# Kernel tuning notes

Measured on AMD Instinct MI355X. Metric: run time of the kernel, lower is better.

Reference implementation:

```python
import jax, jax.numpy as jnp
import numpy as np

TAYLOR_ORDER = 16      # Taylor terms after scaling (||A_s|| <= 0.5 -> machine precision)
MAX_SQUARINGS = 16     # fixed upper bound on squaring steps (jit-friendly)


def batched_expm(A):
    """Vectorized scaling-and-squaring matrix exponential for A of shape [..., n, n].

    Replaces the original per-item torch.linalg.matrix_exp Python loop with one
    fused batched computation (same math: exp(Q*t)).
    """
    n = A.shape[-1]
    I = jnp.eye(n, dtype=A.dtype)
    # per-matrix infinity norm [...,]
    nrm = jnp.max(jnp.sum(jnp.abs(A), axis=-1), axis=-1)
    # number of squarings so that scaled norm <= 0.5
    s = jnp.clip(jnp.ceil(jnp.log2(jnp.maximum(nrm, 1e-30) / 0.5)), 0.0, float(MAX_SQUARINGS))
    As = A * jnp.exp2(-s)[..., None, None]
    # Taylor series: P = I + As + As^2/2! + ...
    P = jnp.broadcast_to(I, A.shape)
    term = P
    for k in range(1, TAYLOR_ORDER + 1):
        term = jnp.matmul(term, As) / k
        P = P + term
    # undo scaling: square s times (data-dependent count via masked squaring)
    s_b = s[..., None, None]
    for i in range(MAX_SQUARINGS):
        P = jnp.where(s_b > i, jnp.matmul(P, P), P)
    return P


def setup_inputs() -> dict:
    key = jax.random.key(0)
    k1, k2 = jax.random.split(key)
    rate_matrix = jax.random.normal(k1, (64, 32768, 4, 4), dtype=jnp.float32)
    time = jax.random.uniform(k2, (64,), dtype=jnp.float32)
    return {"rate_matrix": rate_matrix, "time": time}


def reference(rate_matrix, time):
    # Qt = rate_matrix[i, j] * time[i], batched over (batch, seq_len)
    Qt = rate_matrix * time[:, None, None, None]
    return batched_expm(Qt)  # [B, S, 4, 4] transition probability matrices
```

## Files before the change

### kernel.cpp

```cpp
#include <hip/hip_runtime.h>
#include <math.h>


typedef float f4 __attribute__((ext_vector_type(4)));

constexpr int NMAT = 2;
constexpr int TPB  = 256;
constexpr int MPB  = NMAT * TPB;

__device__ __forceinline__ void mm4(float* __restrict__ D,
                                    const float* __restrict__ X,
                                    const float* __restrict__ Y)
{
    #pragma unroll
    for (int i = 0; i < 4; ++i) {
        const float x0 = X[4*i+0], x1 = X[4*i+1];
        const float x2 = X[4*i+2], x3 = X[4*i+3];
        #pragma unroll
        for (int j = 0; j < 4; ++j) {
            float v = x0 * Y[j];
            v = __builtin_fmaf(x1, Y[4+j],  v);
            v = __builtin_fmaf(x2, Y[8+j],  v);
            v = __builtin_fmaf(x3, Y[12+j], v);
            D[4*i+j] = v;
        }
    }
}

__device__ __forceinline__ void expm4_one(const f4 r[4], float t, f4 o[4])
{
    const float at = fabsf(t);
    float nrm = 0.0f;
    #pragma unroll
    for (int i = 0; i < 4; ++i) {
        float rs = fabsf(r[i].x) + fabsf(r[i].y) + fabsf(r[i].z) + fabsf(r[i].w);
        nrm = fmaxf(nrm, rs);
    }
    nrm *= at;

    float sf = ceilf(log2f(fmaxf(nrm, 1e-30f) * 2.0f));
    sf = fminf(fmaxf(sf, 0.0f), 16.0f);
    const int   si = (int)sf;
    const float c  = t * exp2f(-sf);

    float a[16];
    #pragma unroll
    for (int i = 0; i < 4; ++i) {
        a[4*i+0] = r[i].x * c;
        a[4*i+1] = r[i].y * c;
        a[4*i+2] = r[i].z * c;
        a[4*i+3] = r[i].w * c;
    }

    float A2[16], A3[16];
    mm4(A2, a, a);
    mm4(A3, A2, a);

    constexpr float C2 = 1.0f/2.0f,     C3 = 1.0f/6.0f;
    constexpr float C4 = 1.0f/24.0f,    C5 = 1.0f/120.0f;
    constexpr float C6 = 1.0f/720.0f,   C7 = 1.0f/5040.0f;
    constexpr float C8 = 1.0f/40320.0f, C9 = 1.0f/362880.0f;

    float G[16], HI[16], PI[16];
    #pragma unroll
    for (int i = 0; i < 16; ++i) {
        G[i]  = __builtin_fmaf(C9, A3[i],
                __builtin_fmaf(C8, A2[i], C7 * a[i]));
        HI[i] = __builtin_fmaf(C5, A2[i], C4 * a[i]);
        PI[i] = __builtin_fmaf(C2, A2[i], a[i]);
    }
    G[0]  += C6; G[5]  += C6; G[10] += C6; G[15] += C6;
    HI[0] += C3; HI[5] += C3; HI[10] += C3; HI[15] += C3;
    PI[0] += 1.0f; PI[5] += 1.0f; PI[10] += 1.0f; PI[15] += 1.0f;

    float H[16];
    #pragma unroll
    for (int i = 0; i < 4; ++i) {
        const float g0 = G[4*i+0], g1 = G[4*i+1];
        const float g2 = G[4*i+2], g3 = G[4*i+3];
        #pragma unroll
        for (int j = 0; j < 4; ++j) {
            float v = HI[4*i+j];
            v = __builtin_fmaf(g0, A3[j],    v);
            v = __builtin_fmaf(g1, A3[4+j],  v);
            v = __builtin_fmaf(g2, A3[8+j],  v);
            v = __builtin_fmaf(g3, A3[12+j], v);
            H[4*i+j] = v;
        }
    }

    float P[16];
    #pragma unroll
    for (int i = 0; i < 4; ++i) {
        const float h0 = H[4*i+0], h1 = H[4*i+1];
        const float h2 = H[4*i+2], h3 = H[4*i+3];
        #pragma unroll
        for (int j = 0; j < 4; ++j) {
            float v = PI[4*i+j];
            v = __builtin_fmaf(h0, A3[j],    v);
            v = __builtin_fmaf(h1, A3[4+j],  v);
            v = __builtin_fmaf(h2, A3[8+j],  v);
            v = __builtin_fmaf(h3, A3[12+j], v);
            P[4*i+j] = v;
        }
    }

    int it = si;
    while (it >= 2) {
        float Q[16];
        mm4(Q, P, P);
        mm4(P, Q, Q);
        it -= 2;
    }
    if (it) {
        float Q[16];
        mm4(Q, P, P);
        #pragma unroll
        for (int i = 0; i < 16; ++i) P[i] = Q[i];
    }

    #pragma unroll
    for (int i = 0; i < 4; ++i) {
        f4 v; v.x = P[4*i+0]; v.y = P[4*i+1]; v.z = P[4*i+2]; v.w = P[4*i+3];
        o[i] = v;
    }
}

__global__ void __launch_bounds__(TPB) expm4_kernel(
    const float* __restrict__ A,
    const float* __restrict__ tvec,
    float* __restrict__ out,
    int M, int S, int s_blocks)
{
    const int tid = threadIdx.x;
    const long long mat0 = (long long)blockIdx.x * MPB;
    const long long m0 = mat0 + tid;
    const long long m1 = m0 + TPB;

    float t0, t1;
    if (s_blocks > 0) {
        const float t = tvec[blockIdx.x / s_blocks];
        t0 = t; t1 = t;
    } else {
        t0 = tvec[(int)(m0 / S)];
        t1 = (m1 < M) ? tvec[(int)(m1 / S)] : 0.0f;
    }

    const f4* Ap = reinterpret_cast<const f4*>(A);
    f4 r0[4], r1[4];
    const bool v0 = (m0 < M), v1 = (m1 < M);
    if (v0) {
        #pragma unroll
        for (int k = 0; k < 4; ++k) r0[k] = Ap[m0 * 4 + k];
    }
    if (v1) {
        #pragma unroll
        for (int k = 0; k < 4; ++k) r1[k] = Ap[m1 * 4 + k];
    }

    f4* Op = reinterpret_cast<f4*>(out);

    if (v0) {
        f4 o[4];
        expm4_one(r0, t0, o);
        #pragma unroll
        for (int k = 0; k < 4; ++k) Op[m0 * 4 + k] = o[k];
    }
    if (v1) {
        f4 o[4];
        expm4_one(r1, t1, o);
        #pragma unroll
        for (int k = 0; k < 4; ++k) Op[m1 * 4 + k] = o[k];
    }
}

extern "C" void kernel_launch(void* const* d_in, const int* in_sizes, int n_in,
                              void* d_out, int out_size, void* d_ws, size_t ws_size,
                              hipStream_t stream) {
    const float* A    = (const float*)d_in[0];
    const float* tvec = (const float*)d_in[1];
    float* out        = (float*)d_out;

    const int B = in_sizes[1];
    const int M = in_sizes[0] / 16;
    const int S = M / B;

    const int s_blocks = (S % MPB == 0) ? (S / MPB) : 0;

    const int blocks = (M + MPB - 1) / MPB;
    expm4_kernel<<<blocks, TPB, 0, stream>>>(A, tvec, out, M, S, s_blocks);
}
```

Before: 237.3 us.

## Use grid-stride loop with register prefetch of next matrix and bit-trick scaling

Replaces the two-matrices-per-thread layout with a grid-stride loop in which each thread handles about four matrices. Each iteration prefetches the next matrix's rows into registers before computing the current one, so load latency overlaps the arithmetic. The squaring count and scale factor are now taken from the float exponent bits instead of log2f/ceilf/exp2f, and launch bounds request six blocks per SM. The prefetch adds register pressure and fewer blocks are launched, which may reduce occupancy or leave tail imbalance.

```diff
diff --git a/kernel.cpp b/kernel.cpp
--- a/kernel.cpp
+++ b/kernel.cpp
@@ -4,9 +4,8 @@
 
 typedef float f4 __attribute__((ext_vector_type(4)));
 
-constexpr int NMAT = 2;
-constexpr int TPB  = 256;
-constexpr int MPB  = NMAT * TPB;
+constexpr int TPB   = 256;
+constexpr int KITER = 4;
 
 __device__ __forceinline__ void mm4(float* __restrict__ D,
                                     const float* __restrict__ X,
@@ -38,10 +37,11 @@
     }
     nrm *= at;
 
-    float sf = ceilf(log2f(fmaxf(nrm, 1e-30f) * 2.0f));
-    sf = fminf(fmaxf(sf, 0.0f), 16.0f);
-    const int   si = (int)sf;
-    const float c  = t * exp2f(-sf);
+    const float    x = fmaxf(nrm, 1e-30f) * 2.0f;
+    const unsigned u = __float_as_uint(x);
+    int si = (int)(u >> 23) - 127 + ((u & 0x7fffffu) != 0u);
+    si = si < 0 ? 0 : (si > 16 ? 16 : si);
+    const float c = t * __uint_as_float((unsigned)(127 - si) << 23);
 
     float a[16];
     #pragma unroll
@@ -126,51 +126,46 @@
     }
 }
 
-__global__ void __launch_bounds__(TPB) expm4_kernel(
+__global__ void __launch_bounds__(TPB, 6) expm4_kernel(
     const float* __restrict__ A,
     const float* __restrict__ tvec,
     float* __restrict__ out,
-    int M, int S, int s_blocks)
+    int M, int S, int sdivb)
 {
-    const int tid = threadIdx.x;
-    const long long mat0 = (long long)blockIdx.x * MPB;
-    const long long m0 = mat0 + tid;
-    const long long m1 = m0 + TPB;
+    const int stride = (int)gridDim.x * TPB;
+    const int m0     = (int)blockIdx.x * TPB + (int)threadIdx.x;
 
-    float t0, t1;
-    if (s_blocks > 0) {
-        const float t = tvec[blockIdx.x / s_blocks];
-        t0 = t; t1 = t;
-    } else {
-        t0 = tvec[(int)(m0 / S)];
-        t1 = (m1 < M) ? tvec[(int)(m1 / S)] : 0.0f;
-    }
+    const f4* __restrict__ Ap = reinterpret_cast<const f4*>(A);
+    f4*       __restrict__ Op = reinterpret_cast<f4*>(out);
 
-    const f4* Ap = reinterpret_cast<const f4*>(A);
-    f4 r0[4], r1[4];
-    const bool v0 = (m0 < M), v1 = (m1 < M);
-    if (v0) {
+    const int mi = m0 < M ? m0 : (M - 1);
+    f4 rc[4];
+    #pragma unroll
+    for (int q = 0; q < 4; ++q) rc[q] = Ap[mi * 4 + q];
+
+    int k = 0;
+    for (int m = m0; m < M; m += stride, ++k) {
+        float t;
+        if (sdivb > 0) {
+            t = tvec[((unsigned)blockIdx.x + (unsigned)k * gridDim.x) / (unsigned)sdivb];
+        } else {
+            t = tvec[m / S];
+        }
+
+        int mn = m + stride;
+        mn = mn < M ? mn : (M - 1);
+        f4 rn0 = Ap[mn * 4 + 0];
+        f4 rn1 = Ap[mn * 4 + 1];
+        f4 rn2 = Ap[mn * 4 + 2];
+        f4 rn3 = Ap[mn * 4 + 3];
+        __builtin_amdgcn_sched_barrier(0);
+
+        f4 o[4];
+        expm4_one(rc, t, o);
         #pragma unroll
-        for (int k = 0; k < 4; ++k) r0[k] = Ap[m0 * 4 + k];
-    }
-    if (v1) {
-        #pragma unroll
-        for (int k = 0; k < 4; ++k) r1[k] = Ap[m1 * 4 + k];
-    }
+        for (int q = 0; q < 4; ++q) Op[m * 4 + q] = o[q];
 
-    f4* Op = reinterpret_cast<f4*>(out);
-
-    if (v0) {
-        f4 o[4];
-        expm4_one(r0, t0, o);
-        #pragma unroll
-        for (int k = 0; k < 4; ++k) Op[m0 * 4 + k] = o[k];
-    }
-    if (v1) {
-        f4 o[4];
-        expm4_one(r1, t1, o);
-        #pragma unroll
-        for (int k = 0; k < 4; ++k) Op[m1 * 4 + k] = o[k];
+        rc[0] = rn0; rc[1] = rn1; rc[2] = rn2; rc[3] = rn3;
     }
 }
 
@@ -185,8 +180,9 @@
     const int M = in_sizes[0] / 16;
     const int S = M / B;
 
-    const int s_blocks = (S % MPB == 0) ? (S / MPB) : 0;
+    const int sdivb = (S % TPB == 0) ? (S / TPB) : 0;
 
-    const int blocks = (M + MPB - 1) / MPB;
-    expm4_kernel<<<blocks, TPB, 0, stream>>>(A, tvec, out, M, S, s_blocks);
+    int blocks = (M + TPB * KITER - 1) / (TPB * KITER);
+    if (blocks < 1) blocks = 1;
+    expm4_kernel<<<blocks, TPB, 0, stream>>>(A, tvec, out, M, S, sdivb);
 }
```

After: 239.6 us. No clear change (+1.0%).
